# Kernel optimization log

Measured on AMD Instinct MI355X. Metric: run time of the kernel, lower is better.

Reference implementation:

```python
import jax, jax.numpy as jnp
import numpy as np

SUB_NO = 20
T_NO = 200
NB = 19            # cos_basis_no
COS_SHIFT = 1.0
COS_SCALE = 5.0
T_DATA = 100000
E_NO = 2000
I_NO = 400


def _cos_basis():
    x = jnp.arange(T_NO, dtype=jnp.float32)
    raw = COS_SCALE * jnp.log(x + COS_SHIFT)                      # [T_no]
    phi = (jnp.pi / 2.0) * jnp.arange(NB, dtype=jnp.float32)[:, None]  # [NB,1]
    basis = 0.5 * jnp.cos(raw[None, :] - phi) + 0.5               # [NB, T_no]
    mask = (raw[None, :] >= phi - jnp.pi) & (raw[None, :] <= phi + jnp.pi)
    return jnp.where(mask, basis, 0.0)


def _gconv(x, kern_flipped):
    # depthwise (grouped) 1d cross-correlation, VALID padding, matching torch F.conv1d
    # x: [L, sub], kern_flipped: [sub, T_no] (already time-flipped) -> [L - T_no + 1, sub]
    out = jax.lax.conv_general_dilated(
        x.T[None],                      # [1, sub, L]
        kern_flipped[:, None, :],       # [sub, 1, T_no]
        window_strides=(1,), padding='VALID',
        feature_group_count=x.shape[1],
        dimension_numbers=('NCH', 'OIH', 'NCH'))
    return out[0].T


def setup_inputs() -> dict:
    key = jax.random.key(0)
    ks = jax.random.split(key, 16)
    rng = np.random.default_rng(0)
    # tree adjacency: each node j>0 has a parent < j; C_den[parent, child] = 1
    C_den = np.zeros((SUB_NO, SUB_NO), np.float32)
    for j in range(1, SUB_NO):
        C_den[rng.integers(0, j), j] = 1.0
    # one-hot synapse -> subunit maps
    C_syn_e = np.zeros((SUB_NO, E_NO), np.float32)
    C_syn_e[rng.integers(0, SUB_NO, E_NO), np.arange(E_NO)] = 1.0
    C_syn_i = np.zeros((SUB_NO, I_NO), np.float32)
    C_syn_i[rng.integers(0, SUB_NO, I_NO), np.arange(I_NO)] = 1.0
    # sparse binary spike trains
    S_e = (jax.random.uniform(ks[0], (T_DATA, E_NO)) < 0.02).astype(jnp.float32)
    S_i = (jax.random.uniform(ks[1], (T_DATA, I_NO)) < 0.02).astype(jnp.float32)
    Z = (jax.random.uniform(ks[2], (T_DATA, SUB_NO)) < 0.05).astype(jnp.float32)
    return {
        'S_e': S_e, 'S_i': S_i, 'Z': Z,
        'C_den': jnp.asarray(C_den), 'C_syn_e': jnp.asarray(C_syn_e), 'C_syn_i': jnp.asarray(C_syn_i),
        'W_syn': 0.1 * jax.random.normal(ks[3], (SUB_NO, NB, 2)),
        'W_hist': 0.1 * jax.random.normal(ks[4], (SUB_NO, NB)),
        'W_spk': jnp.ones(SUB_NO) + 0.05 * jax.random.normal(ks[5], (SUB_NO,)),
        'Delta_spk': jax.random.uniform(ks[6], (SUB_NO,), maxval=2.0),
        'Tau_spk': 3.0 * jnp.ones(SUB_NO) + 0.1 * jax.random.normal(ks[7], (SUB_NO,)),
        'V_o': jax.random.normal(ks[8], (1,)),
        'Theta': 0.1 * jax.random.normal(ks[9], (SUB_NO,)),
        'weight1': 0.1 * jax.random.normal(ks[10], (SUB_NO, 6)),
        'weight2': 0.1 * jax.random.normal(ks[11], (6, 6)),
        'weight3': 0.1 * jax.random.normal(ks[12], (6, SUB_NO)),
    }


def reference(S_e, S_i, Z, C_den, C_syn_e, C_syn_i, W_syn, W_hist, W_spk,
              Delta_spk, Tau_spk, V_o, Theta, weight1, weight2, weight3):
    cb = _cos_basis()                                  # [NB, T_no]
    sub = C_den.shape[0]
    pad = lambda x, n: jnp.concatenate([jnp.zeros((n, sub), x.dtype), x], axis=0)

    # --- spike_convolve ---
    syn_e = S_e @ C_syn_e.T                            # [T, sub]
    syn_i = S_i @ C_syn_i.T
    e_kern = W_syn[:, :, 0] @ cb                       # [sub, T_no]
    i_kern = W_syn[:, :, 1] @ cb
    filtered_e = _gconv(pad(syn_e, T_NO - 1), jnp.flip(e_kern, 1))
    filtered_i = _gconv(pad(syn_i, T_NO - 1), jnp.flip(i_kern, 1))
    syn = filtered_e + filtered_i                      # [T, sub]

    # --- history and spike kernels (causal, 1-step delayed: pad T_no, drop last) ---
    hist_kern = W_hist @ cb                            # [sub, T_no]
    pad_Z = pad(Z, T_NO)                               # [T + T_no, sub]
    hist_filt = _gconv(pad_Z, jnp.flip(hist_kern, 1))[:-1]   # [T, sub]

    t = jnp.maximum(jnp.arange(T_NO, dtype=jnp.float32)[None, :] - Delta_spk[:, None], 0.0)
    t_tau = t / (Tau_spk[:, None] ** 2)
    spk_kern = t_tau * jnp.exp(-t_tau) * (W_spk[:, None] ** 2)  # [sub, T_no]
    spk_filt = _gconv(pad_Z, jnp.flip(spk_kern, 1))[:-1]        # [T, sub]

    # --- per-subunit loop, vectorized: leaf gather == spk_filt @ C_den.T ---
    sub_in = syn + Theta[None, :] + hist_filt + spk_filt @ C_den.T   # [T, sub]
    h0 = jax.nn.leaky_relu(sub_in)
    h1 = jax.nn.leaky_relu(h0[:, :, None] * weight1[None, :, :])     # [T, sub, 6]
    h2 = jax.nn.leaky_relu(jnp.einsum('tsk,kj->tsj', h1, weight2))   # [T, sub, 6]
    final_Z = jax.nn.sigmoid(jnp.einsum('tsj,js->ts', h2, weight3))  # [T, sub]

    final_V = spk_filt[:, 0] + V_o[0]                  # [T]
    out_filters = jnp.concatenate([e_kern, i_kern, hist_kern, spk_kern], axis=0)  # [4*sub, T_no]
    return final_V, final_Z, out_filters
```

## Files before the change

kernel.cpp:

```cpp
#include <hip/hip_runtime.h>

typedef unsigned short ushort_t;
typedef unsigned int uint_t;

#define T_DATA 100000
#define E_NO 2000
#define I_NO 400
#define SUB 20
#define TNO 200
#define NBASIS 19
#define HEAD 256
#define TAILPAD 2048
#define SIGSTRIDE (HEAD + T_DATA + TAILPAD)
#define TILE 2048
#define RPT 8
#define TSPAN 32
#define ACCSTR 36

#define OFF_Z  ((size_t)T_DATA)
#define OFF_F  ((size_t)T_DATA + (size_t)T_DATA*SUB)

__device__ __forceinline__ float b2f(ushort_t u) {
    union { uint_t i; float f; } v; v.i = ((uint_t)u) << 16; return v.f;
}
__device__ __forceinline__ ushort_t f2b(float f) {
    union { uint_t i; float f_; } v; v.f_ = f;
    uint_t b = v.i;
    uint_t r = (b + 0x7FFFu + ((b >> 16) & 1u)) >> 16;
    return (ushort_t)r;
}
__device__ __forceinline__ float ldin(const void* p, size_t idx, int mode) {
    return mode ? b2f(((const ushort_t*)p)[idx]) : ((const float*)p)[idx];
}
__device__ __forceinline__ void stout(void* p, size_t idx, float val, int mode) {
    if (mode) ((ushort_t*)p)[idx] = f2b(val);
    else      ((float*)p)[idx] = val;
}
__device__ __forceinline__ float f4get(const float4& v, int i) {
    return i == 0 ? v.x : i == 1 ? v.y : i == 2 ? v.z : v.w;
}
__device__ __forceinline__ float pick12(const float4& L, const float4& M, const float4& H, int e) {
    return e < 4 ? f4get(L, e) : e < 8 ? f4get(M, e - 4) : f4get(H, e - 8);
}

__global__ void k_probe(const void* tau, int* flag) {
    if (threadIdx.x == 0) {
        const ushort_t* tu = (const ushort_t*)tau;
        int cnt = 0;
        for (int i = 0; i < 20; ++i) {
            float v = b2f(tu[i]);
            if (v >= 1.5f && v < 6.0f) cnt++;
        }
        *flag = (cnt >= 15) ? 1 : 0;
    }
}

__global__ __launch_bounds__(256) void k0_prep(
        const int* __restrict__ flag,
        const void* Csyn_e, const void* Csyn_i,
        const void* W_syn, const void* W_hist,
        const void* W_spk, const void* Delta, const void* Tau,
        float* ws_f, int* mape, int* mapi, ushort_t* sigs, void* dout) {
    int mode = *flag;
    int bid = blockIdx.x, tid = threadIdx.x;
    if (bid < 80) {
        int kidx = bid / 20, s = bid % 20;
        int tau = tid;
        if (tau < TNO) {
            float val;
            if (kidx < 3) {
                float raw = 5.0f * logf((float)tau + 1.0f);
                val = 0.f;
                for (int b = 0; b < NBASIS; ++b) {
                    float phi = 1.5707963267948966f * (float)b;
                    float d = raw - phi;
                    float basis = (d >= -3.14159265358979f && d <= 3.14159265358979f)
                                  ? (0.5f * cosf(d) + 0.5f) : 0.f;
                    float w = (kidx == 0) ? ldin(W_syn, (size_t)s * NBASIS * 2 + b * 2 + 0, mode)
                            : (kidx == 1) ? ldin(W_syn, (size_t)s * NBASIS * 2 + b * 2 + 1, mode)
                                          : ldin(W_hist, (size_t)s * NBASIS + b, mode);
                    val += w * basis;
                }
            } else {
                float dl = ldin(Delta, s, mode), tu = ldin(Tau, s, mode), wk = ldin(W_spk, s, mode);
                float t = fmaxf((float)tau - dl, 0.f);
                float tt = t / (tu * tu);
                val = tt * expf(-tt) * (wk * wk);
            }
            ws_f[kidx * 4000 + s * TNO + tau] = val;
            stout(dout, OFF_F + (size_t)bid * TNO + tau, val, mode);
        }
    } else if (bid < 96) {
        int e = (bid - 80) * 256 + tid;
        if (e < E_NO) {
            int m = 0;
            for (int s = 0; s < SUB; ++s)
                if (ldin(Csyn_e, (size_t)s * E_NO + e, mode) != 0.f) { m = s; break; }
            mape[e] = m;
        }
    } else if (bid < 98) {
        int e = (bid - 96) * 256 + tid;
        if (e < I_NO) {
            int m = 0;
            for (int s = 0; s < SUB; ++s)
                if (ldin(Csyn_i, (size_t)s * I_NO + e, mode) != 0.f) { m = s; break; }
            mapi[e] = m;
        }
    } else if (bid < 158) {
        int rg = bid - 98;
        int sg = rg / 20, s = rg % 20;
        ushort_t* p = sigs + (size_t)sg * SUB * SIGSTRIDE + (size_t)s * SIGSTRIDE;
        for (int i = tid; i < HEAD; i += 256) p[i] = 0;
        for (int i = tid; i < TAILPAD; i += 256) p[HEAD + T_DATA + i] = 0;
    }
}

__global__ __launch_bounds__(256) void k1_reduce(
        const int* __restrict__ flag,
        const void* __restrict__ S_e, const void* __restrict__ S_i,
        const void* __restrict__ Z,
        const int* __restrict__ mape, const int* __restrict__ mapi,
        ushort_t* __restrict__ sigs) {
    __shared__ int me[E_NO];
    __shared__ int mi[I_NO];
    __shared__ float acc[60 * ACCSTR];
    int tid = threadIdx.x;
    int mode = *flag;
    for (int i = tid; i < E_NO; i += 256) me[i] = mape[i];
    for (int i = tid; i < I_NO; i += 256) mi[i] = mapi[i];
    for (int i = tid; i < 60 * ACCSTR; i += 256) acc[i] = 0.f;
    __syncthreads();

    int base = blockIdx.x * TSPAN;
    for (int rl = 0; rl < TSPAN; ++rl) {
        int row = base + rl;
        if (mode) {
            if (tid < 250) {
                uint4 u = *(const uint4*)((const ushort_t*)S_e + (size_t)row * E_NO + tid * 8);
                uint_t wd[4] = {u.x, u.y, u.z, u.w};
                #pragma unroll
                for (int q = 0; q < 4; ++q) {
                    float a = b2f((ushort_t)(wd[q] & 0xFFFF));
                    float b = b2f((ushort_t)(wd[q] >> 16));
                    if (a != 0.f) atomicAdd(&acc[me[tid * 8 + 2 * q] * ACCSTR + rl], a);
                    if (b != 0.f) atomicAdd(&acc[me[tid * 8 + 2 * q + 1] * ACCSTR + rl], b);
                }
            }
            if (tid < 50) {
                uint4 u = *(const uint4*)((const ushort_t*)S_i + (size_t)row * I_NO + tid * 8);
                uint_t wd[4] = {u.x, u.y, u.z, u.w};
                #pragma unroll
                for (int q = 0; q < 4; ++q) {
                    float a = b2f((ushort_t)(wd[q] & 0xFFFF));
                    float b = b2f((ushort_t)(wd[q] >> 16));
                    if (a != 0.f) atomicAdd(&acc[(20 + mi[tid * 8 + 2 * q]) * ACCSTR + rl], a);
                    if (b != 0.f) atomicAdd(&acc[(20 + mi[tid * 8 + 2 * q + 1]) * ACCSTR + rl], b);
                }
            }
        } else {
            if (tid < 250) {
                const float* pe = (const float*)S_e + (size_t)row * E_NO;
                float4 u0 = *(const float4*)(pe + tid * 4);
                float4 u1 = *(const float4*)(pe + (tid + 250) * 4);
                float v0[4] = {u0.x, u0.y, u0.z, u0.w};
                float v1[4] = {u1.x, u1.y, u1.z, u1.w};
                #pragma unroll
                for (int q = 0; q < 4; ++q) {
                    if (v0[q] != 0.f) atomicAdd(&acc[me[tid * 4 + q] * ACCSTR + rl], v0[q]);
                    if (v1[q] != 0.f) atomicAdd(&acc[me[(tid + 250) * 4 + q] * ACCSTR + rl], v1[q]);
                }
            }
            if (tid < 100) {
                float4 u = *(const float4*)((const float*)S_i + (size_t)row * I_NO + tid * 4);
                float v[4] = {u.x, u.y, u.z, u.w};
                #pragma unroll
                for (int q = 0; q < 4; ++q)
                    if (v[q] != 0.f) atomicAdd(&acc[(20 + mi[tid * 4 + q]) * ACCSTR + rl], v[q]);
            }
        }
        if (tid >= 192 && tid < 212) {
            int s = tid - 192;
            acc[(40 + s) * ACCSTR + rl] = ldin(Z, (size_t)row * SUB + s, mode);
        }
    }
    __syncthreads();

    for (int idx = tid; idx < 60 * (TSPAN / 4); idx += 256) {
        int sig = idx >> 3;
        int g = idx & 7;
        int t0 = g * 4;
        const float* src = &acc[sig * ACCSTR + t0];
        float4 v = *(const float4*)src;
        uint2 o;
        o.x = (uint_t)f2b(v.x) | ((uint_t)f2b(v.y) << 16);
        o.y = (uint_t)f2b(v.z) | ((uint_t)f2b(v.w) << 16);
        *(uint2*)(sigs + (size_t)sig * SIGSTRIDE + HEAD + base + t0) = o;
    }
}

__global__ __launch_bounds__(256) void k2_conv(
        const ushort_t* __restrict__ sigs, const float* __restrict__ ws_f,
        ushort_t* __restrict__ base_out, ushort_t* __restrict__ spk_out) {
    __shared__ float X[3 * 2248 + 800];
    float* XE = X;
    float* XI = X + 2248;
    float* ZZ = X + 4496;
    float* KK = X + 6744;
    int s = blockIdx.y;
    int t0 = blockIdx.x * TILE;
    int tid = threadIdx.x;

    for (int k = 0; k < 4; ++k)
        for (int j = tid; j < TNO; j += 256)
            KK[k * TNO + j] = ws_f[k * 4000 + s * TNO + j];

    {
        const ushort_t* g0 = sigs + (size_t)s * SIGSTRIDE + (HEAD - 200) + t0;
        const ushort_t* g1 = g0 + (size_t)SUB * SIGSTRIDE;
        const ushort_t* g2 = g0 + (size_t)2 * SUB * SIGSTRIDE;
        for (int v = tid; v < 281; v += 256) {
            uint4 u = *(const uint4*)(g0 + v * 8);
            float* d = XE + v * 8;
            d[0]=b2f((ushort_t)(u.x&0xFFFF)); d[1]=b2f((ushort_t)(u.x>>16));
            d[2]=b2f((ushort_t)(u.y&0xFFFF)); d[3]=b2f((ushort_t)(u.y>>16));
            d[4]=b2f((ushort_t)(u.z&0xFFFF)); d[5]=b2f((ushort_t)(u.z>>16));
            d[6]=b2f((ushort_t)(u.w&0xFFFF)); d[7]=b2f((ushort_t)(u.w>>16));
        }
        for (int v = tid; v < 281; v += 256) {
            uint4 u = *(const uint4*)(g1 + v * 8);
            float* d = XI + v * 8;
            d[0]=b2f((ushort_t)(u.x&0xFFFF)); d[1]=b2f((ushort_t)(u.x>>16));
            d[2]=b2f((ushort_t)(u.y&0xFFFF)); d[3]=b2f((ushort_t)(u.y>>16));
            d[4]=b2f((ushort_t)(u.z&0xFFFF)); d[5]=b2f((ushort_t)(u.z>>16));
            d[6]=b2f((ushort_t)(u.w&0xFFFF)); d[7]=b2f((ushort_t)(u.w>>16));
        }
        for (int v = tid; v < 281; v += 256) {
            uint4 u = *(const uint4*)(g2 + v * 8);
            float* d = ZZ + v * 8;
            d[0]=b2f((ushort_t)(u.x&0xFFFF)); d[1]=b2f((ushort_t)(u.x>>16));
            d[2]=b2f((ushort_t)(u.y&0xFFFF)); d[3]=b2f((ushort_t)(u.y>>16));
            d[4]=b2f((ushort_t)(u.z&0xFFFF)); d[5]=b2f((ushort_t)(u.z>>16));
            d[6]=b2f((ushort_t)(u.w&0xFFFF)); d[7]=b2f((ushort_t)(u.w>>16));
        }
    }
    __syncthreads();

    float acc[RPT] = {0,0,0,0,0,0,0,0};
    float spk[RPT] = {0,0,0,0,0,0,0,0};
    const float4* XE4 = (const float4*)XE;
    const float4* XI4 = (const float4*)XI;
    const float4* ZZ4 = (const float4*)ZZ;
    const float4* KE4 = (const float4*)(KK);
    const float4* KI4 = (const float4*)(KK + 200);
    const float4* KH4 = (const float4*)(KK + 400);
    const float4* KS4 = (const float4*)(KK + 600);
    int w4 = 2 * tid + 49;
    float4 eL = XE4[w4], eM = XE4[w4 + 1], eH = XE4[w4 + 2];
    float4 iL = XI4[w4], iM = XI4[w4 + 1], iH = XI4[w4 + 2];
    float4 zL = ZZ4[w4], zM = ZZ4[w4 + 1], zH = ZZ4[w4 + 2];

    for (int c = 0; c < 50; ++c) {
        if (c > 0) {
            eH = eM; eM = eL; eL = XE4[w4 - c];
            iH = iM; iM = iL; iL = XI4[w4 - c];
            zH = zM; zM = zL; zL = ZZ4[w4 - c];
        }
        float4 ke = KE4[c], ki = KI4[c], kh = KH4[c], ks = KS4[c];
        #pragma unroll
        for (int u = 0; u < 4; ++u) {
            float keu = f4get(ke, u), kiu = f4get(ki, u);
            float khu = f4get(kh, u), ksu = f4get(ks, u);
            #pragma unroll
            for (int r = 0; r < RPT; ++r) {
                float xe = pick12(eL, eM, eH, 4 + r - u);
                float xi = pick12(iL, iM, iH, 4 + r - u);
                float zz = pick12(zL, zM, zH, 3 + r - u);
                acc[r] += keu * xe;
                acc[r] += kiu * xi;
                acc[r] += khu * zz;
                spk[r] += ksu * zz;
            }
        }
    }
    int tbase = t0 + RPT * tid;
    if (tbase + RPT <= T_DATA) {
        uint4 pb, pq;
        pb.x = (uint_t)f2b(acc[0]) | ((uint_t)f2b(acc[1]) << 16);
        pb.y = (uint_t)f2b(acc[2]) | ((uint_t)f2b(acc[3]) << 16);
        pb.z = (uint_t)f2b(acc[4]) | ((uint_t)f2b(acc[5]) << 16);
        pb.w = (uint_t)f2b(acc[6]) | ((uint_t)f2b(acc[7]) << 16);
        pq.x = (uint_t)f2b(spk[0]) | ((uint_t)f2b(spk[1]) << 16);
        pq.y = (uint_t)f2b(spk[2]) | ((uint_t)f2b(spk[3]) << 16);
        pq.z = (uint_t)f2b(spk[4]) | ((uint_t)f2b(spk[5]) << 16);
        pq.w = (uint_t)f2b(spk[6]) | ((uint_t)f2b(spk[7]) << 16);
        *(uint4*)(base_out + (size_t)s * T_DATA + tbase) = pb;
        *(uint4*)(spk_out + (size_t)s * T_DATA + tbase) = pq;
    } else {
        #pragma unroll
        for (int r = 0; r < RPT; ++r) {
            int t = tbase + r;
            if (t < T_DATA) {
                base_out[(size_t)s * T_DATA + t] = f2b(acc[r]);
                spk_out[(size_t)s * T_DATA + t] = f2b(spk[r]);
            }
        }
    }
}

__global__ __launch_bounds__(256) void k3_mlp(
        const int* __restrict__ flag,
        const ushort_t* __restrict__ base_out, const ushort_t* __restrict__ spk_out,
        const void* __restrict__ C_den, const void* __restrict__ Theta,
        const void* __restrict__ Vo,
        const void* __restrict__ w1, const void* __restrict__ w2,
        const void* __restrict__ w3,
        void* __restrict__ dout) {
    __shared__ float cd[400], th[20], W1[120], W2[36], W3[120];
    __shared__ float vo;
    int tid = threadIdx.x;
    int mode = *flag;
    for (int i = tid; i < 400; i += 256) cd[i] = ldin(C_den, i, mode);
    if (tid < 20) th[tid] = ldin(Theta, tid, mode);
    if (tid < 120) W1[tid] = ldin(w1, tid, mode);
    if (tid < 36) W2[tid] = ldin(w2, tid, mode);
    if (tid >= 128 && tid < 248) W3[tid - 128] = ldin(w3, tid - 128, mode);
    if (tid == 0) vo = ldin(Vo, 0, mode);
    __syncthreads();
    int t = blockIdx.x * 256 + tid;
    if (t >= T_DATA) return;
    float sv[20], bv[20];
    #pragma unroll
    for (int c = 0; c < 20; ++c) {
        sv[c] = b2f(spk_out[(size_t)c * T_DATA + t]);
        bv[c] = b2f(base_out[(size_t)c * T_DATA + t]);
    }
    stout(dout, (size_t)t, sv[0] + vo, mode);
    #pragma unroll
    for (int p = 0; p < 20; ++p) {
        float ps = 0.f;
        #pragma unroll
        for (int c = 0; c < 20; ++c) ps += cd[p * 20 + c] * sv[c];
        float x = bv[p] + th[p] + ps;
        float h0 = x >= 0.f ? x : 0.01f * x;
        float h1[6];
        #pragma unroll
        for (int k = 0; k < 6; ++k) {
            float y = h0 * W1[p * 6 + k];
            h1[k] = y >= 0.f ? y : 0.01f * y;
        }
        float zacc = 0.f;
        #pragma unroll
        for (int j = 0; j < 6; ++j) {
            float a = 0.f;
            #pragma unroll
            for (int k = 0; k < 6; ++k) a += h1[k] * W2[k * 6 + j];
            float h2 = a >= 0.f ? a : 0.01f * a;
            zacc += h2 * W3[j * 20 + p];
        }
        float zv = 1.f / (1.f + expf(-zacc));
        stout(dout, OFF_Z + (size_t)t * SUB + p, zv, mode);
    }
}

extern "C" void kernel_launch(void* const* d_in, const int* in_sizes, int n_in,
                              void* d_out, int out_size, void* d_ws, size_t ws_size,
                              hipStream_t stream) {
    const void* S_e     = d_in[0];
    const void* S_i     = d_in[1];
    const void* Z       = d_in[2];
    const void* C_den   = d_in[3];
    const void* C_syn_e = d_in[4];
    const void* C_syn_i = d_in[5];
    const void* W_syn   = d_in[6];
    const void* W_hist  = d_in[7];
    const void* W_spk   = d_in[8];
    const void* Delta   = d_in[9];
    const void* Tau     = d_in[10];
    const void* Vo      = d_in[11];
    const void* Theta   = d_in[12];
    const void* w1      = d_in[13];
    const void* w2      = d_in[14];
    const void* w3      = d_in[15];

    char* w = (char*)d_ws;
    int*      flag     = (int*)w;
    float*    ws_f     = (float*)(w + 64);
    int*      mape     = (int*)(w + 64 + 64000);
    int*      mapi     = (int*)(w + 64 + 64000 + 8000);
    ushort_t* sigs     = (ushort_t*)(w + 73664);
    ushort_t* base_out = (ushort_t*)(w + 12350144);
    ushort_t* spk_out  = (ushort_t*)(w + 16350144);

    hipLaunchKernelGGL(k_probe, dim3(1), dim3(64), 0, stream, Tau, flag);
    hipLaunchKernelGGL(k0_prep, dim3(158), dim3(256), 0, stream,
                       flag, C_syn_e, C_syn_i, W_syn, W_hist, W_spk, Delta, Tau,
                       ws_f, mape, mapi, sigs, d_out);
    hipLaunchKernelGGL(k1_reduce, dim3(T_DATA / TSPAN), dim3(256), 0, stream,
                       flag, S_e, S_i, Z, mape, mapi, sigs);
    hipLaunchKernelGGL(k2_conv, dim3((T_DATA + TILE - 1) / TILE, SUB), dim3(256), 0, stream,
                       sigs, ws_f, base_out, spk_out);
    hipLaunchKernelGGL(k3_mlp, dim3((T_DATA + 255) / 256), dim3(256), 0, stream,
                       flag, base_out, spk_out, C_den, Theta, Vo, w1, w2, w3, d_out);
}
```

Measured before the change: 299.8 us.

## Replace atomic synapse scatter with bf16 MFMA matmul against pre-swizzled C_syn tables

In bf16 mode, the per-subunit synaptic reduction is now a dense matmul S_e·C_syn_eᵀ and S_i·C_syn_iᵀ using 32x32x16 bf16 MFMA instructions. The C_syn tables are pre-swizzled into an MFMA operand layout during prep. This replaces the shared-memory atomicAdd scatter, and each block now covers 128 rows instead of 32. The separate probe kernel is removed, with every kernel detecting the dtype mode inline. The cost is redundant multiplies on mostly-zero data and 20/32 lane utilisation of the N dimension.

```diff
diff --git a/kernel.cpp b/kernel.cpp
--- a/kernel.cpp
+++ b/kernel.cpp
@@ -2,6 +2,9 @@
 
 typedef unsigned short ushort_t;
 typedef unsigned int uint_t;
+typedef float __attribute__((ext_vector_type(4))) f32x4;
+typedef float __attribute__((ext_vector_type(16))) f32x16;
+typedef short __attribute__((ext_vector_type(8))) short8_t;
 
 #define T_DATA 100000
 #define E_NO 2000
@@ -10,12 +13,12 @@
 #define TNO 200
 #define NBASIS 19
 #define HEAD 256
-#define TAILPAD 2048
+#define TAILPAD 384
 #define SIGSTRIDE (HEAD + T_DATA + TAILPAD)
 #define TILE 2048
 #define RPT 8
-#define TSPAN 32
-#define ACCSTR 36
+#define MROWS 128
+#define CLSTR 132
 
 #define OFF_Z  ((size_t)T_DATA)
 #define OFF_F  ((size_t)T_DATA + (size_t)T_DATA*SUB)
@@ -42,27 +45,27 @@
 __device__ __forceinline__ float pick12(const float4& L, const float4& M, const float4& H, int e) {
     return e < 4 ? f4get(L, e) : e < 8 ? f4get(M, e - 4) : f4get(H, e - 8);
 }
-
-__global__ void k_probe(const void* tau, int* flag) {
-    if (threadIdx.x == 0) {
-        const ushort_t* tu = (const ushort_t*)tau;
-        int cnt = 0;
-        for (int i = 0; i < 20; ++i) {
-            float v = b2f(tu[i]);
-            if (v >= 1.5f && v < 6.0f) cnt++;
-        }
-        *flag = (cnt >= 15) ? 1 : 0;
-    }
+__device__ __forceinline__ int detect_mode(const void* tau) {
+    const ushort_t* tu = (const ushort_t*)tau;
+    int cnt = 0;
+    #pragma unroll
+    for (int i = 0; i < 20; ++i) {
+        float v = b2f(tu[i]);
+        if (v >= 1.5f && v < 6.0f) cnt++;
+    }
+    return (cnt >= 15) ? 1 : 0;
 }
 
 __global__ __launch_bounds__(256) void k0_prep(
-        const int* __restrict__ flag,
         const void* Csyn_e, const void* Csyn_i,
         const void* W_syn, const void* W_hist,
         const void* W_spk, const void* Delta, const void* Tau,
-        float* ws_f, int* mape, int* mapi, ushort_t* sigs, void* dout) {
-    int mode = *flag;
+        float* ws_f, int* mape, int* mapi, ushort_t* Btab, ushort_t* sigs, void* dout) {
+    __shared__ int smode;
     int bid = blockIdx.x, tid = threadIdx.x;
+    if (tid == 0) smode = detect_mode(Tau);
+    __syncthreads();
+    int mode = smode;
     if (bid < 80) {
         int kidx = bid / 20, s = bid % 20;
         int tau = tid;
@@ -112,89 +115,160 @@
         ushort_t* p = sigs + (size_t)sg * SUB * SIGSTRIDE + (size_t)s * SIGSTRIDE;
         for (int i = tid; i < HEAD; i += 256) p[i] = 0;
         for (int i = tid; i < TAILPAD; i += 256) p[HEAD + T_DATA + i] = 0;
+    } else if (bid < 233) {
+        int idx0 = (bid - 158) * 1024 + tid * 4;
+        #pragma unroll
+        for (int q = 0; q < 4; ++q) {
+            int idx = idx0 + q;
+            ushort_t out;
+            if (idx < 64000) {
+                int kstep = idx >> 9;
+                int lane = (idx >> 3) & 63;
+                int j = idx & 7;
+                int n = lane & 31;
+                int k = kstep * 16 + ((lane >> 5) << 3) + j;
+                float v = (n < SUB) ? ldin(Csyn_e, (size_t)n * E_NO + k, mode) : 0.f;
+                out = f2b(v);
+            } else {
+                int i2 = idx - 64000;
+                int kstep = i2 >> 9;
+                int lane = (i2 >> 3) & 63;
+                int j = i2 & 7;
+                int n = lane & 31;
+                int k = kstep * 16 + ((lane >> 5) << 3) + j;
+                float v = (n < SUB) ? ldin(Csyn_i, (size_t)n * I_NO + k, mode) : 0.f;
+                out = f2b(v);
+            }
+            Btab[idx] = out;
+        }
     }
 }
 
 __global__ __launch_bounds__(256) void k1_reduce(
-        const int* __restrict__ flag,
         const void* __restrict__ S_e, const void* __restrict__ S_i,
         const void* __restrict__ Z,
         const int* __restrict__ mape, const int* __restrict__ mapi,
+        const ushort_t* __restrict__ Btab,
+        const void* __restrict__ Tau,
         ushort_t* __restrict__ sigs) {
-    __shared__ int me[E_NO];
-    __shared__ int mi[I_NO];
-    __shared__ float acc[60 * ACCSTR];
+    __shared__ float CL[60 * CLSTR];
+    __shared__ int smode;
     int tid = threadIdx.x;
-    int mode = *flag;
-    for (int i = tid; i < E_NO; i += 256) me[i] = mape[i];
-    for (int i = tid; i < I_NO; i += 256) mi[i] = mapi[i];
-    for (int i = tid; i < 60 * ACCSTR; i += 256) acc[i] = 0.f;
-    __syncthreads();
-
-    int base = blockIdx.x * TSPAN;
-    for (int rl = 0; rl < TSPAN; ++rl) {
-        int row = base + rl;
-        if (mode) {
+    if (tid == 0) smode = detect_mode(Tau);
+    __syncthreads();
+    int mode = smode;
+    int Mbase = blockIdx.x * MROWS;
+    int lane = tid & 63, wave = tid >> 6;
+
+    {
+        int nvalid = (T_DATA - Mbase) * SUB;
+        if (nvalid > MROWS * SUB) nvalid = MROWS * SUB;
+        for (int e = tid * 4; e + 3 < nvalid; e += 1024) {
+            float z0, z1, z2, z3;
+            if (mode) {
+                uint2 u = *(const uint2*)((const ushort_t*)Z + (size_t)Mbase * SUB + e);
+                z0 = b2f((ushort_t)(u.x & 0xFFFF)); z1 = b2f((ushort_t)(u.x >> 16));
+                z2 = b2f((ushort_t)(u.y & 0xFFFF)); z3 = b2f((ushort_t)(u.y >> 16));
+            } else {
+                f32x4 u = *(const f32x4*)((const float*)Z + (size_t)Mbase * SUB + e);
+                z0 = u[0]; z1 = u[1]; z2 = u[2]; z3 = u[3];
+            }
+            CL[(40 + (e + 0) % SUB) * CLSTR + (e + 0) / SUB] = z0;
+            CL[(40 + (e + 1) % SUB) * CLSTR + (e + 1) / SUB] = z1;
+            CL[(40 + (e + 2) % SUB) * CLSTR + (e + 2) / SUB] = z2;
+            CL[(40 + (e + 3) % SUB) * CLSTR + (e + 3) / SUB] = z3;
+        }
+    }
+
+    if (mode) {
+        int waveRow0 = Mbase + wave * 32;
+        bool wvalid = (waveRow0 < T_DATA);
+        int row = waveRow0 + (lane & 31);
+        int rowc = wvalid ? row : 0;
+        const ushort_t* Se = (const ushort_t*)S_e;
+        const ushort_t* Si = (const ushort_t*)S_i;
+        const ushort_t* pa  = Se + (size_t)rowc * E_NO + ((lane >> 5) << 3);
+        const ushort_t* pb  = Btab + lane * 8;
+        const ushort_t* pai = Si + (size_t)rowc * I_NO + ((lane >> 5) << 3);
+        const ushort_t* pbi = Btab + 64000 + lane * 8;
+
+        f32x16 accE, accI;
+        #pragma unroll
+        for (int r = 0; r < 16; ++r) { accE[r] = 0.f; accI[r] = 0.f; }
+
+        #pragma unroll 5
+        for (int ks = 0; ks < 125; ++ks) {
+            short8_t av = *(const short8_t*)(pa + ks * 16);
+            short8_t bv = *(const short8_t*)(pb + ks * 512);
+            accE = __builtin_amdgcn_mfma_f32_32x32x16_bf16(av, bv, accE, 0, 0, 0);
+        }
+        #pragma unroll 5
+        for (int ks = 0; ks < 25; ++ks) {
+            short8_t av = *(const short8_t*)(pai + ks * 16);
+            short8_t bv = *(const short8_t*)(pbi + ks * 512);
+            accI = __builtin_amdgcn_mfma_f32_32x32x16_bf16(av, bv, accI, 0, 0, 0);
+        }
+
+        int s = lane & 31;
+        if (wvalid && s < SUB) {
+            int thi = wave * 32 + ((lane >> 5) << 2);
+            #pragma unroll
+            for (int r = 0; r < 16; ++r) {
+                int tloc = thi + (r & 3) + ((r >> 2) << 3);
+                CL[s * CLSTR + tloc] = accE[r];
+                CL[(20 + s) * CLSTR + tloc] = accI[r];
+            }
+        }
+    } else {
+        for (int i = tid; i < 40 * CLSTR; i += 256) CL[i] = 0.f;
+        __syncthreads();
+        int be[8], bi8[8];
+        if (tid < 250) {
+            #pragma unroll
+            for (int j = 0; j < 4; ++j) be[j] = mape[tid * 4 + j] * CLSTR;
+            #pragma unroll
+            for (int j = 0; j < 4; ++j) be[4 + j] = mape[(tid + 250) * 4 + j] * CLSTR;
+        }
+        if (tid < 100) {
+            #pragma unroll
+            for (int j = 0; j < 4; ++j) bi8[j] = (20 + mapi[tid * 4 + j]) * CLSTR;
+        }
+        const float* Sef = (const float*)S_e;
+        const float* Sif = (const float*)S_i;
+        for (int rl = 0; rl < MROWS; ++rl) {
+            int row = Mbase + rl;
+            if (row >= T_DATA) break;
             if (tid < 250) {
-                uint4 u = *(const uint4*)((const ushort_t*)S_e + (size_t)row * E_NO + tid * 8);
-                uint_t wd[4] = {u.x, u.y, u.z, u.w};
+                const float* pe = Sef + (size_t)row * E_NO;
+                f32x4 a = *(const f32x4*)(pe + tid * 4);
+                f32x4 b = *(const f32x4*)(pe + (tid + 250) * 4);
                 #pragma unroll
                 for (int q = 0; q < 4; ++q) {
-                    float a = b2f((ushort_t)(wd[q] & 0xFFFF));
-                    float b = b2f((ushort_t)(wd[q] >> 16));
-                    if (a != 0.f) atomicAdd(&acc[me[tid * 8 + 2 * q] * ACCSTR + rl], a);
-                    if (b != 0.f) atomicAdd(&acc[me[tid * 8 + 2 * q + 1] * ACCSTR + rl], b);
+                    if (a[q] != 0.f) atomicAdd(&CL[be[q] + rl], a[q]);
+                    if (b[q] != 0.f) atomicAdd(&CL[be[4 + q] + rl], b[q]);
                 }
             }
-            if (tid < 50) {
-                uint4 u = *(const uint4*)((const ushort_t*)S_i + (size_t)row * I_NO + tid * 8);
-                uint_t wd[4] = {u.x, u.y, u.z, u.w};
-                #pragma unroll
-                for (int q = 0; q < 4; ++q) {
-                    float a = b2f((ushort_t)(wd[q] & 0xFFFF));
-                    float b = b2f((ushort_t)(wd[q] >> 16));
-                    if (a != 0.f) atomicAdd(&acc[(20 + mi[tid * 8 + 2 * q]) * ACCSTR + rl], a);
-                    if (b != 0.f) atomicAdd(&acc[(20 + mi[tid * 8 + 2 * q + 1]) * ACCSTR + rl], b);
-                }
-            }
-        } else {
-            if (tid < 250) {
-                const float* pe = (const float*)S_e + (size_t)row * E_NO;
-                float4 u0 = *(const float4*)(pe + tid * 4);
-                float4 u1 = *(const float4*)(pe + (tid + 250) * 4);
-                float v0[4] = {u0.x, u0.y, u0.z, u0.w};
-                float v1[4] = {u1.x, u1.y, u1.z, u1.w};
-                #pragma unroll
-                for (int q = 0; q < 4; ++q) {
-                    if (v0[q] != 0.f) atomicAdd(&acc[me[tid * 4 + q] * ACCSTR + rl], v0[q]);
-                    if (v1[q] != 0.f) atomicAdd(&acc[me[(tid + 250) * 4 + q] * ACCSTR + rl], v1[q]);
-                }
-            }
             if (tid < 100) {
-                float4 u = *(const float4*)((const float*)S_i + (size_t)row * I_NO + tid * 4);
-                float v[4] = {u.x, u.y, u.z, u.w};
+                f32x4 c = *(const f32x4*)(Sif + (size_t)row * I_NO + tid * 4);
                 #pragma unroll
                 for (int q = 0; q < 4; ++q)
-                    if (v[q] != 0.f) atomicAdd(&acc[(20 + mi[tid * 4 + q]) * ACCSTR + rl], v[q]);
-            }
-        }
-        if (tid >= 192 && tid < 212) {
-            int s = tid - 192;
-            acc[(40 + s) * ACCSTR + rl] = ldin(Z, (size_t)row * SUB + s, mode);
-        }
-    }
-    __syncthreads();
-
-    for (int idx = tid; idx < 60 * (TSPAN / 4); idx += 256) {
-        int sig = idx >> 3;
-        int g = idx & 7;
+                    if (c[q] != 0.f) atomicAdd(&CL[bi8[q] + rl], c[q]);
+            }
+        }
+    }
+    __syncthreads();
+
+    for (int idx = tid; idx < 60 * (MROWS / 4); idx += 256) {
+        int sig = idx >> 5;
+        int g = idx & 31;
         int t0 = g * 4;
-        const float* src = &acc[sig * ACCSTR + t0];
+        if (Mbase + t0 >= T_DATA) continue;
+        const float* src = &CL[sig * CLSTR + t0];
         float4 v = *(const float4*)src;
         uint2 o;
         o.x = (uint_t)f2b(v.x) | ((uint_t)f2b(v.y) << 16);
         o.y = (uint_t)f2b(v.z) | ((uint_t)f2b(v.w) << 16);
-        *(uint2*)(sigs + (size_t)sig * SIGSTRIDE + HEAD + base + t0) = o;
+        *(uint2*)(sigs + (size_t)sig * SIGSTRIDE + HEAD + Mbase + t0) = o;
     }
 }
 
@@ -308,17 +382,20 @@
 }
 
 __global__ __launch_bounds__(256) void k3_mlp(
-        const int* __restrict__ flag,
         const ushort_t* __restrict__ base_out, const ushort_t* __restrict__ spk_out,
         const void* __restrict__ C_den, const void* __restrict__ Theta,
         const void* __restrict__ Vo,
         const void* __restrict__ w1, const void* __restrict__ w2,
         const void* __restrict__ w3,
+        const void* __restrict__ Tau,
         void* __restrict__ dout) {
     __shared__ float cd[400], th[20], W1[120], W2[36], W3[120];
     __shared__ float vo;
+    __shared__ int smode;
     int tid = threadIdx.x;
-    int mode = *flag;
+    if (tid == 0) smode = detect_mode(Tau);
+    __syncthreads();
+    int mode = smode;
     for (int i = tid; i < 400; i += 256) cd[i] = ldin(C_den, i, mode);
     if (tid < 20) th[tid] = ldin(Theta, tid, mode);
     if (tid < 120) W1[tid] = ldin(w1, tid, mode);
@@ -383,22 +460,21 @@
     const void* w3      = d_in[15];
 
     char* w = (char*)d_ws;
-    int*      flag     = (int*)w;
     float*    ws_f     = (float*)(w + 64);
-    int*      mape     = (int*)(w + 64 + 64000);
-    int*      mapi     = (int*)(w + 64 + 64000 + 8000);
-    ushort_t* sigs     = (ushort_t*)(w + 73664);
-    ushort_t* base_out = (ushort_t*)(w + 12350144);
-    ushort_t* spk_out  = (ushort_t*)(w + 16350144);
-
-    hipLaunchKernelGGL(k_probe, dim3(1), dim3(64), 0, stream, Tau, flag);
-    hipLaunchKernelGGL(k0_prep, dim3(158), dim3(256), 0, stream,
-                       flag, C_syn_e, C_syn_i, W_syn, W_hist, W_spk, Delta, Tau,
-                       ws_f, mape, mapi, sigs, d_out);
-    hipLaunchKernelGGL(k1_reduce, dim3(T_DATA / TSPAN), dim3(256), 0, stream,
-                       flag, S_e, S_i, Z, mape, mapi, sigs);
+    int*      mape     = (int*)(w + 64064);
+    int*      mapi     = (int*)(w + 72064);
+    ushort_t* Btab     = (ushort_t*)(w + 73664);
+    ushort_t* sigs     = (ushort_t*)(w + 227264);
+    ushort_t* base_out = (ushort_t*)(w + 12304064);
+    ushort_t* spk_out  = (ushort_t*)(w + 16304064);
+
+    hipLaunchKernelGGL(k0_prep, dim3(233), dim3(256), 0, stream,
+                       C_syn_e, C_syn_i, W_syn, W_hist, W_spk, Delta, Tau,
+                       ws_f, mape, mapi, Btab, sigs, d_out);
+    hipLaunchKernelGGL(k1_reduce, dim3((T_DATA + MROWS - 1) / MROWS), dim3(256), 0, stream,
+                       S_e, S_i, Z, mape, mapi, Btab, Tau, sigs);
     hipLaunchKernelGGL(k2_conv, dim3((T_DATA + TILE - 1) / TILE, SUB), dim3(256), 0, stream,
                        sigs, ws_f, base_out, spk_out);
     hipLaunchKernelGGL(k3_mlp, dim3((T_DATA + 255) / 256), dim3(256), 0, stream,
-                       flag, base_out, spk_out, C_den, Theta, Vo, w1, w2, w3, d_out);
-}
+                       base_out, spk_out, C_den, Theta, Vo, w1, w2, w3, Tau, d_out);
+}
```

After: 321.0 us. +7.1%, slower.
